# Kernel optimization log

Hardware: AMD Instinct MI355X
Metric: run time of the kernel (lower is better)

The kernel has to match this reference:

```python
import jax, jax.numpy as jnp
import numpy as np

EMB = 1024
HID = 1024
COMB = 2 * HID  # bidirectional encoder
BATCH = 16384


def _lin(x, W, b):
    # x: [B, in], W: [in, out], b: [out]
    return x @ W + b


def setup_inputs() -> dict:
    key = jax.random.key(0)
    ks = jax.random.split(key, 30)
    s = 0.02
    d = {
        "in_word": jax.random.normal(ks[0], (BATCH, EMB), jnp.float32),
        "last_hid_state": jax.random.normal(ks[1], (BATCH, HID), jnp.float32),
        "attended_state": jax.random.normal(ks[2], (BATCH, COMB), jnp.float32),
    }
    names_shapes = [
        ("W", (EMB, HID)), ("Wz", (EMB, HID)), ("Wr", (EMB, HID)),
        ("U", (HID, HID)), ("Uz", (HID, HID)), ("Ur", (HID, HID)),
        ("C", (COMB, HID)), ("Cz", (COMB, HID)), ("Cr", (COMB, HID)),
        ("Uo", (HID, HID)), ("Vo", (EMB, HID)), ("Co", (COMB, HID)),
    ]
    for i, (n, sh) in enumerate(names_shapes):
        d[n] = jax.random.normal(ks[3 + i], sh, jnp.float32) * s
        d["b" + n.lower()] = jnp.zeros((HID,), jnp.float32)
    return d


def reference(in_word, last_hid_state, attended_state,
              W, bw, Wz, bwz, Wr, bwr,
              U, bu, Uz, buz, Ur, bur,
              C, bc, Cz, bcz, Cr, bcr,
              Uo, buo, Vo, bvo, Co, bco):
    z = jax.nn.sigmoid(_lin(in_word, Wz, bwz) + _lin(last_hid_state, Uz, buz)
                       + _lin(attended_state, Cz, bcz))
    r = jax.nn.sigmoid(_lin(in_word, Wr, bwr) + _lin(last_hid_state, Ur, bur)
                       + _lin(attended_state, Cr, bcr))
    s_tilda = jnp.tanh(_lin(in_word, W, bw) + _lin(r * last_hid_state, U, bu)
                       + _lin(attended_state, C, bc))
    s = (1.0 - z) * last_hid_state + z * s_tilda
    t_i = jax.nn.relu(_lin(s, Uo, buo) + _lin(in_word, Vo, bvo)
                      + _lin(attended_state, Co, bco))
    return (s, t_i)
```

## Files before the change

kernel.cpp:

```cpp
#include <hip/hip_runtime.h>
#include <stdint.h>
#include <stddef.h>


#define MODE_Z 0
#define MODE_R 1
#define MODE_S 2
#define MODE_T 3

typedef __attribute__((ext_vector_type(8))) __bf16 bf16x8;
typedef __attribute__((ext_vector_type(4))) float f32x4;
typedef __attribute__((ext_vector_type(8))) unsigned short us8;

__device__ __forceinline__ unsigned short f2bf(float f) {
  union { float f; unsigned u; } v; v.f = f;
  unsigned r = 0x7FFFu + ((v.u >> 16) & 1u);
  return (unsigned short)((v.u + r) >> 16);
}
__device__ __forceinline__ float bf2f(unsigned short h) {
  union { unsigned u; float f; } v; v.u = ((unsigned)h) << 16;
  return v.f;
}

__device__ __forceinline__ void gload_lds16(const unsigned short* g, unsigned short* l) {
  __builtin_amdgcn_global_load_lds(
      (const __attribute__((address_space(1))) void*)g,
      (__attribute__((address_space(3))) void*)l, 16, 0, 0);
}

__global__ void cvt_xh(const float* __restrict__ x, const float* __restrict__ h,
                       unsigned short* __restrict__ xb, unsigned short* __restrict__ hb) {
  const size_t NX = 16777216;
  size_t i = ((size_t)blockIdx.x * 256 + threadIdx.x) * 8;
  const float* s; unsigned short* d; size_t off;
  if (i < NX) { s = x; d = xb; off = i; } else { s = h; d = hb; off = i - NX; }
  f32x4 v0 = *(const f32x4*)(s + off);
  f32x4 v1 = *(const f32x4*)(s + off + 4);
  us8 p = { f2bf(v0.x), f2bf(v0.y), f2bf(v0.z), f2bf(v0.w),
            f2bf(v1.x), f2bf(v1.y), f2bf(v1.z), f2bf(v1.w) };
  *(us8*)(d + off) = p;
}

__global__ void cvt_a(const float* __restrict__ a, unsigned short* __restrict__ ab) {
  size_t i = ((size_t)blockIdx.x * 256 + threadIdx.x) * 8;
  f32x4 v0 = *(const f32x4*)(a + i);
  f32x4 v1 = *(const f32x4*)(a + i + 4);
  us8 p = { f2bf(v0.x), f2bf(v0.y), f2bf(v0.z), f2bf(v0.w),
            f2bf(v1.x), f2bf(v1.y), f2bf(v1.z), f2bf(v1.w) };
  *(us8*)(ab + i) = p;
}

struct TArgs {
  const float* src[12];
  unsigned short* dst[12];
};

__global__ void transpose_all(TArgs ta) {
  __shared__ float tile[32][33];
  int t = blockIdx.x;
  int w, K, local;
  if (t < 8192) { w = t >> 10; K = 1024; local = t & 1023; }
  else { int t2 = t - 8192; w = 8 + (t2 >> 11); K = 2048; local = t2 & 2047; }
  int kb = (K == 1024) ? ((local & 31) << 5) : ((local & 63) << 5);
  int nb = (K == 1024) ? ((local >> 5) << 5) : ((local >> 6) << 5);
  const float* src = ta.src[w];
  unsigned short* dst = ta.dst[w];
  int tx = threadIdx.x, ty = threadIdx.y;
  #pragma unroll
  for (int i = 0; i < 32; i += 8)
    tile[ty + i][tx] = src[(size_t)(kb + ty + i) * 1024 + nb + tx];
  __syncthreads();
  #pragma unroll
  for (int i = 0; i < 32; i += 8)
    dst[(size_t)(nb + ty + i) * K + kb + tx] = f2bf(tile[tx][ty + i]);
}

template <int MODE>
__global__ __launch_bounds__(256, 4)
void gemm_fused(const unsigned short* __restrict__ A0,
                const unsigned short* __restrict__ A1,
                const unsigned short* __restrict__ A2,
                const unsigned short* __restrict__ B0T,
                const unsigned short* __restrict__ B1T,
                const unsigned short* __restrict__ B2T,
                const float* __restrict__ b0,
                const float* __restrict__ b1,
                const float* __restrict__ b2,
                const unsigned short* __restrict__ hb,
                const unsigned short* __restrict__ zb,
                float* __restrict__ outf,
                unsigned short* __restrict__ outb) {
  __shared__ unsigned short As[128 * 64];
  __shared__ unsigned short Bs[128 * 64];

  const int tid = threadIdx.x;
  const int bid = blockIdx.x;
  const int xcd = bid & 7;
  const int j8 = bid >> 3;
  const int mBlk = xcd * 16 + (j8 >> 3);
  const int nBlk = j8 & 7;
  const int rowBase = mBlk * 128;
  const int colBase = nBlk * 128;
  const int wave = tid >> 6;
  const int lane = tid & 63;
  const int waveM = wave >> 1;
  const int waveN = wave & 1;
  const int quad = lane >> 4;
  const int lm = lane & 15;
  const int wbase = tid & 192;

  f32x4 acc[4][4];
  #pragma unroll
  for (int i = 0; i < 4; ++i)
    #pragma unroll
    for (int j = 0; j < 4; ++j)
      acc[i][j] = (f32x4){0.f, 0.f, 0.f, 0.f};

  const unsigned short* Asegs[3] = {A0, A1, A2};
  const unsigned short* Bsegs[3] = {B0T, B1T, B2T};

  #pragma unroll
  for (int seg = 0; seg < 3; ++seg) {
    const int K = (seg == 2) ? 2048 : 1024;
    const unsigned short* Ap = Asegs[seg] + (size_t)rowBase * K;
    const unsigned short* Bp = Bsegs[seg] + (size_t)colBase * K;
    const int nChunks = K >> 6;
    for (int kc = 0; kc < nChunks; ++kc) {
      #pragma unroll
      for (int t = 0; t < 4; ++t) {
        int idx = t * 256 + tid;
        int row = idx >> 3;
        int kg = (idx & 7) ^ (row & 7);
        gload_lds16(Ap + (size_t)row * K + (kc << 6) + (kg << 3),
                    &As[(size_t)(t * 256 + wbase) << 3]);
      }
      #pragma unroll
      for (int t = 0; t < 4; ++t) {
        int idx = t * 256 + tid;
        int row = idx >> 3;
        int kg = (idx & 7) ^ (row & 7);
        gload_lds16(Bp + (size_t)row * K + (kc << 6) + (kg << 3),
                    &Bs[(size_t)(t * 256 + wbase) << 3]);
      }
      __syncthreads();
      #pragma unroll
      for (int ks = 0; ks < 2; ++ks) {
        bf16x8 av[4], bv[4];
        #pragma unroll
        for (int i = 0; i < 4; ++i) {
          int r = waveM * 64 + i * 16 + lm;
          int slot = (ks * 4 + quad) ^ (r & 7);
          av[i] = *(const bf16x8*)&As[(r << 6) + (slot << 3)];
        }
        #pragma unroll
        for (int j = 0; j < 4; ++j) {
          int c = waveN * 64 + j * 16 + lm;
          int slot = (ks * 4 + quad) ^ (c & 7);
          bv[j] = *(const bf16x8*)&Bs[(c << 6) + (slot << 3)];
        }
        #pragma unroll
        for (int i = 0; i < 4; ++i)
          #pragma unroll
          for (int j = 0; j < 4; ++j)
            acc[i][j] = __builtin_amdgcn_mfma_f32_16x16x32_bf16(av[i], bv[j], acc[i][j], 0, 0, 0);
      }
      __syncthreads();
    }
  }

  #pragma unroll
  for (int j = 0; j < 4; ++j) {
    const int col = colBase + waveN * 64 + j * 16 + lm;
    const float bias = b0[col] + b1[col] + b2[col];
    #pragma unroll
    for (int i = 0; i < 4; ++i) {
      #pragma unroll
      for (int r = 0; r < 4; ++r) {
        const int row = rowBase + waveM * 64 + i * 16 + quad * 4 + r;
        const size_t idx = (size_t)row * 1024 + col;
        float v = acc[i][j][r] + bias;
        if constexpr (MODE == MODE_Z) {
          outb[idx] = f2bf(1.f / (1.f + __expf(-v)));
        } else if constexpr (MODE == MODE_R) {
          float rv = 1.f / (1.f + __expf(-v));
          outb[idx] = f2bf(rv * bf2f(hb[idx]));
        } else if constexpr (MODE == MODE_S) {
          float avv = fabsf(v);
          float e = __expf(-2.f * avv);
          float st = (1.f - e) / (1.f + e);
          st = v < 0.f ? -st : st;
          float zv = bf2f(zb[idx]);
          float hv = bf2f(hb[idx]);
          float s = (1.f - zv) * hv + zv * st;
          outf[idx] = s;
          outb[idx] = f2bf(s);
        } else {
          outf[idx] = v > 0.f ? v : 0.f;
        }
      }
    }
  }
}

extern "C" void kernel_launch(void* const* d_in, const int* in_sizes, int n_in,
                              void* d_out, int out_size, void* d_ws, size_t ws_size,
                              hipStream_t stream) {
  (void)in_sizes; (void)n_in; (void)out_size; (void)ws_size;
  const float* x  = (const float*)d_in[0];
  const float* h  = (const float*)d_in[1];
  const float* a  = (const float*)d_in[2];
  const float* W   = (const float*)d_in[3];  const float* bw  = (const float*)d_in[4];
  const float* Wz  = (const float*)d_in[5];  const float* bwz = (const float*)d_in[6];
  const float* Wr  = (const float*)d_in[7];  const float* bwr = (const float*)d_in[8];
  const float* U   = (const float*)d_in[9];  const float* bu  = (const float*)d_in[10];
  const float* Uz  = (const float*)d_in[11]; const float* buz = (const float*)d_in[12];
  const float* Ur  = (const float*)d_in[13]; const float* bur = (const float*)d_in[14];
  const float* C   = (const float*)d_in[15]; const float* bc  = (const float*)d_in[16];
  const float* Cz  = (const float*)d_in[17]; const float* bcz = (const float*)d_in[18];
  const float* Cr  = (const float*)d_in[19]; const float* bcr = (const float*)d_in[20];
  const float* Uo  = (const float*)d_in[21]; const float* buo = (const float*)d_in[22];
  const float* Vo  = (const float*)d_in[23]; const float* bvo = (const float*)d_in[24];
  const float* Co  = (const float*)d_in[25]; const float* bco = (const float*)d_in[26];

  const size_t M1 = 1024u * 1024u;
  unsigned short* wsb = (unsigned short*)d_ws;
  unsigned short* WzT = wsb + 0 * M1;
  unsigned short* UzT = wsb + 1 * M1;
  unsigned short* WrT = wsb + 2 * M1;
  unsigned short* UrT = wsb + 3 * M1;
  unsigned short* WT  = wsb + 4 * M1;
  unsigned short* UT  = wsb + 5 * M1;
  unsigned short* VoT = wsb + 6 * M1;
  unsigned short* UoT = wsb + 7 * M1;
  unsigned short* CzT = wsb + 8 * M1;
  unsigned short* CrT = wsb + 10 * M1;
  unsigned short* CT  = wsb + 12 * M1;
  unsigned short* CoT = wsb + 14 * M1;
  unsigned short* x_bf = wsb + 16 * M1;

  unsigned short* h_bf = (unsigned short*)((float*)d_out + 16 * M1);
  unsigned short* a_bf = (unsigned short*)d_in[0];
  unsigned short* rh   = (unsigned short*)d_in[1];
  unsigned short* z_bf = (unsigned short*)d_in[1] + 16 * M1;
  unsigned short* s_bf = (unsigned short*)d_in[2];

  float* s_out = (float*)d_out;
  float* t_out = (float*)d_out + 16 * M1;

  cvt_xh<<<16384, 256, 0, stream>>>(x, h, x_bf, h_bf);
  cvt_a<<<16384, 256, 0, stream>>>(a, a_bf);
  TArgs ta;
  const float* wsrc[12] = {Wz, Uz, Wr, Ur, W, U, Vo, Uo, Cz, Cr, C, Co};
  unsigned short* wdst[12] = {WzT, UzT, WrT, UrT, WT, UT, VoT, UoT, CzT, CrT, CT, CoT};
  for (int i = 0; i < 12; ++i) { ta.src[i] = wsrc[i]; ta.dst[i] = wdst[i]; }
  transpose_all<<<16384, dim3(32, 8), 0, stream>>>(ta);

  dim3 g(1024), b(256);
  gemm_fused<MODE_R><<<g, b, 0, stream>>>(x_bf, h_bf, a_bf, WrT, UrT, CrT,
                                          bwr, bur, bcr, h_bf, nullptr, nullptr, rh);
  gemm_fused<MODE_Z><<<g, b, 0, stream>>>(x_bf, h_bf, a_bf, WzT, UzT, CzT,
                                          bwz, buz, bcz, nullptr, nullptr, nullptr, z_bf);
  gemm_fused<MODE_S><<<g, b, 0, stream>>>(x_bf, rh, a_bf, WT, UT, CT,
                                          bw, bu, bc, h_bf, z_bf, s_out, s_bf);
  gemm_fused<MODE_T><<<g, b, 0, stream>>>(x_bf, s_bf, a_bf, VoT, UoT, CoT,
                                          bvo, buo, bco, nullptr, nullptr, t_out, nullptr);
}
```

Measured before the change: 1.048 ms.

## Rewrite fused GEMM as 256x256 tile, 8-wave double-buffered pipelined kernel

Replaces the 128x128, 4-wave GEMM with a 256x256 output tile per 512-thread block. K-chunks are double-buffered in 128KB of LDS, and global-to-LDS loads for later chunks are interleaved with quadrant MFMA groups under raw s_barrier and vmcnt waits. MFMA sections are wrapped in raised wave priority. The aim is to hide load latency and raise arithmetic intensity per LDS byte. The cost is a grid of only 256 blocks at one block per CU, plus more register pressure from 128 accumulator floats per lane.

Result: slower. 1.532 ms (+46.1%).

```diff
diff --git a/kernel.cpp b/kernel.cpp
--- a/kernel.cpp
+++ b/kernel.cpp
@@ -75,8 +75,13 @@
     dst[(size_t)(nb + ty + i) * K + kb + tx] = f2bf(tile[tx][ty + i]);
 }
 
+#define BARRIER() asm volatile("s_barrier" ::: "memory")
+#define WAIT_VM(N) asm volatile("s_waitcnt vmcnt(" #N ")" ::: "memory")
+#define PRIO1() __builtin_amdgcn_s_setprio(1)
+#define PRIO0() __builtin_amdgcn_s_setprio(0)
+
 template <int MODE>
-__global__ __launch_bounds__(256, 4)
+__global__ __launch_bounds__(512, 2)
 void gemm_fused(const unsigned short* __restrict__ A0,
                 const unsigned short* __restrict__ A1,
                 const unsigned short* __restrict__ A2,
@@ -90,112 +95,161 @@
                 const unsigned short* __restrict__ zb,
                 float* __restrict__ outf,
                 unsigned short* __restrict__ outb) {
-  __shared__ unsigned short As[128 * 64];
-  __shared__ unsigned short Bs[128 * 64];
+  __shared__ unsigned short lds_s[65536];
 
   const int tid = threadIdx.x;
   const int bid = blockIdx.x;
-  const int xcd = bid & 7;
-  const int j8 = bid >> 3;
-  const int mBlk = xcd * 16 + (j8 >> 3);
-  const int nBlk = j8 & 7;
-  const int rowBase = mBlk * 128;
-  const int colBase = nBlk * 128;
-  const int wave = tid >> 6;
-  const int lane = tid & 63;
-  const int waveM = wave >> 1;
-  const int waveN = wave & 1;
-  const int quad = lane >> 4;
-  const int lm = lane & 15;
-  const int wbase = tid & 192;
-
-  f32x4 acc[4][4];
+  const int swz = (bid & 7) * 32 + (bid >> 3);
+  const int mBlk = swz >> 2;
+  const int nBlk = swz & 3;
+  const int rowBase = mBlk << 8;
+  const int colBase = nBlk << 8;
+
+  const int l = tid & 63;
+  const int w = tid >> 6;
+  const int wm = w >> 2;
+  const int wn = w & 3;
+  const int lm = l & 15;
+  const int quad = l >> 4;
+
+  f32x4 acc[4][4][2];
   #pragma unroll
-  for (int i = 0; i < 4; ++i)
-    #pragma unroll
-    for (int j = 0; j < 4; ++j)
-      acc[i][j] = (f32x4){0.f, 0.f, 0.f, 0.f};
-
-  const unsigned short* Asegs[3] = {A0, A1, A2};
-  const unsigned short* Bsegs[3] = {B0T, B1T, B2T};
+  for (int q = 0; q < 4; ++q)
+    #pragma unroll
+    for (int fr = 0; fr < 4; ++fr)
+      #pragma unroll
+      for (int fc = 0; fc < 2; ++fc)
+        acc[q][fr][fc] = (f32x4){0.f, 0.f, 0.f, 0.f};
+
+  bf16x8 aF[4][2];
+  bf16x8 bLo[2][2];
+  bf16x8 bHi[2][2];
+
+  auto STAGE = [&](int kt, int op, int half) {
+    const unsigned short* base;
+    int K, kloc;
+    if (kt < 16)      { base = op ? B0T : A0; K = 1024; kloc = kt << 6; }
+    else if (kt < 32) { base = op ? B1T : A1; K = 1024; kloc = (kt - 16) << 6; }
+    else              { base = op ? B2T : A2; K = 2048; kloc = (kt - 32) << 6; }
+    const int rb = (op ? colBase : rowBase) + (half << 7);
+    const unsigned short* g = base + (size_t)rb * K + kloc;
+    unsigned short* lb = lds_s + ((kt & 1) << 15) + (op << 14) + (half << 13);
+    #pragma unroll
+    for (int j = 0; j < 2; ++j) {
+      const int idx = (j << 9) + tid;
+      const int row = idx >> 3;
+      const int kg = (idx & 7) ^ (row & 7);
+      gload_lds16(g + (size_t)row * K + (kg << 3),
+                  lb + ((idx & ~63) << 3));
+    }
+  };
+
+  auto LOAD_A = [&](int cb, int h) {
+    #pragma unroll
+    for (int fr = 0; fr < 4; ++fr) {
+      const int r = wm * 64 + h * 128 + fr * 16 + lm;
+      #pragma unroll
+      for (int ks = 0; ks < 2; ++ks) {
+        const int slot = ((ks << 2) | quad) ^ (lm & 7);
+        aF[fr][ks] = *(const bf16x8*)(lds_s + cb + (r << 6) + (slot << 3));
+      }
+    }
+  };
+  auto LOAD_B = [&](int cb, int h, bf16x8 (&bv)[2][2]) {
+    #pragma unroll
+    for (int fc = 0; fc < 2; ++fc) {
+      const int c = wn * 32 + h * 128 + fc * 16 + lm;
+      #pragma unroll
+      for (int ks = 0; ks < 2; ++ks) {
+        const int slot = ((ks << 2) | quad) ^ (lm & 7);
+        bv[fc][ks] = *(const bf16x8*)(lds_s + cb + 16384 + (c << 6) + (slot << 3));
+      }
+    }
+  };
+  auto MFMA16 = [&](f32x4 (&aq)[4][2], bf16x8 (&bv)[2][2]) {
+    #pragma unroll
+    for (int ks = 0; ks < 2; ++ks)
+      #pragma unroll
+      for (int fr = 0; fr < 4; ++fr)
+        #pragma unroll
+        for (int fc = 0; fc < 2; ++fc)
+          aq[fr][fc] = __builtin_amdgcn_mfma_f32_16x16x32_bf16(
+              aF[fr][ks], bv[fc][ks], aq[fr][fc], 0, 0, 0);
+  };
+
+  STAGE(0, 0, 0); STAGE(0, 1, 0); STAGE(0, 1, 1); STAGE(0, 0, 1);
+  STAGE(1, 0, 0); STAGE(1, 1, 0); STAGE(1, 1, 1);
+  WAIT_VM(6);
+  BARRIER();
+
+  #pragma unroll 1
+  for (int i = 0; i < 31; ++i) {
+    const int t1 = 2 * i + 1, t2 = 2 * i + 2, t3 = 2 * i + 3;
+    LOAD_A(0, 0); LOAD_B(0, 0, bLo); STAGE(t1, 0, 1);
+    BARRIER(); PRIO1(); MFMA16(acc[0], bLo); PRIO0(); BARRIER();
+    LOAD_B(0, 1, bHi); STAGE(t2, 0, 0);
+    BARRIER(); PRIO1(); MFMA16(acc[1], bHi); PRIO0(); BARRIER();
+    LOAD_A(0, 1); STAGE(t2, 1, 0);
+    BARRIER(); PRIO1(); MFMA16(acc[2], bLo); PRIO0(); BARRIER();
+    STAGE(t2, 1, 1);
+    BARRIER(); PRIO1(); MFMA16(acc[3], bHi); PRIO0(); WAIT_VM(6); BARRIER();
+    LOAD_A(32768, 0); LOAD_B(32768, 0, bLo); STAGE(t2, 0, 1);
+    BARRIER(); PRIO1(); MFMA16(acc[0], bLo); PRIO0(); BARRIER();
+    LOAD_B(32768, 1, bHi); STAGE(t3, 0, 0);
+    BARRIER(); PRIO1(); MFMA16(acc[1], bHi); PRIO0(); BARRIER();
+    LOAD_A(32768, 1); STAGE(t3, 1, 0);
+    BARRIER(); PRIO1(); MFMA16(acc[2], bLo); PRIO0(); BARRIER();
+    STAGE(t3, 1, 1);
+    BARRIER(); PRIO1(); MFMA16(acc[3], bHi); PRIO0(); WAIT_VM(6); BARRIER();
+  }
+  LOAD_A(0, 0); LOAD_B(0, 0, bLo); STAGE(63, 0, 1);
+  BARRIER(); PRIO1(); MFMA16(acc[0], bLo); PRIO0(); BARRIER();
+  LOAD_B(0, 1, bHi);
+  BARRIER(); PRIO1(); MFMA16(acc[1], bHi); PRIO0(); BARRIER();
+  LOAD_A(0, 1);
+  BARRIER(); PRIO1(); MFMA16(acc[2], bLo); PRIO0(); BARRIER();
+  BARRIER(); PRIO1(); MFMA16(acc[3], bHi); PRIO0(); WAIT_VM(0); BARRIER();
+  LOAD_A(32768, 0); LOAD_B(32768, 0, bLo);
+  BARRIER(); PRIO1(); MFMA16(acc[0], bLo); PRIO0(); BARRIER();
+  LOAD_B(32768, 1, bHi);
+  BARRIER(); PRIO1(); MFMA16(acc[1], bHi); PRIO0(); BARRIER();
+  LOAD_A(32768, 1);
+  BARRIER(); PRIO1(); MFMA16(acc[2], bLo); PRIO0(); BARRIER();
+  BARRIER(); PRIO1(); MFMA16(acc[3], bHi); PRIO0();
 
   #pragma unroll
-  for (int seg = 0; seg < 3; ++seg) {
-    const int K = (seg == 2) ? 2048 : 1024;
-    const unsigned short* Ap = Asegs[seg] + (size_t)rowBase * K;
-    const unsigned short* Bp = Bsegs[seg] + (size_t)colBase * K;
-    const int nChunks = K >> 6;
-    for (int kc = 0; kc < nChunks; ++kc) {
-      #pragma unroll
-      for (int t = 0; t < 4; ++t) {
-        int idx = t * 256 + tid;
-        int row = idx >> 3;
-        int kg = (idx & 7) ^ (row & 7);
-        gload_lds16(Ap + (size_t)row * K + (kc << 6) + (kg << 3),
-                    &As[(size_t)(t * 256 + wbase) << 3]);
-      }
-      #pragma unroll
-      for (int t = 0; t < 4; ++t) {
-        int idx = t * 256 + tid;
-        int row = idx >> 3;
-        int kg = (idx & 7) ^ (row & 7);
-        gload_lds16(Bp + (size_t)row * K + (kc << 6) + (kg << 3),
-                    &Bs[(size_t)(t * 256 + wbase) << 3]);
-      }
-      __syncthreads();
-      #pragma unroll
-      for (int ks = 0; ks < 2; ++ks) {
-        bf16x8 av[4], bv[4];
+  for (int q = 0; q < 4; ++q) {
+    const int rQ = rowBase + wm * 64 + (q >> 1) * 128;
+    const int cQ = colBase + wn * 32 + (q & 1) * 128;
+    #pragma unroll
+    for (int fc = 0; fc < 2; ++fc) {
+      const int col = cQ + fc * 16 + lm;
+      const float bias = b0[col] + b1[col] + b2[col];
+      #pragma unroll
+      for (int fr = 0; fr < 4; ++fr) {
         #pragma unroll
-        for (int i = 0; i < 4; ++i) {
-          int r = waveM * 64 + i * 16 + lm;
-          int slot = (ks * 4 + quad) ^ (r & 7);
-          av[i] = *(const bf16x8*)&As[(r << 6) + (slot << 3)];
-        }
-        #pragma unroll
-        for (int j = 0; j < 4; ++j) {
-          int c = waveN * 64 + j * 16 + lm;
-          int slot = (ks * 4 + quad) ^ (c & 7);
-          bv[j] = *(const bf16x8*)&Bs[(c << 6) + (slot << 3)];
-        }
-        #pragma unroll
-        for (int i = 0; i < 4; ++i)
-          #pragma unroll
-          for (int j = 0; j < 4; ++j)
-            acc[i][j] = __builtin_amdgcn_mfma_f32_16x16x32_bf16(av[i], bv[j], acc[i][j], 0, 0, 0);
-      }
-      __syncthreads();
-    }
-  }
-
-  #pragma unroll
-  for (int j = 0; j < 4; ++j) {
-    const int col = colBase + waveN * 64 + j * 16 + lm;
-    const float bias = b0[col] + b1[col] + b2[col];
-    #pragma unroll
-    for (int i = 0; i < 4; ++i) {
-      #pragma unroll
-      for (int r = 0; r < 4; ++r) {
-        const int row = rowBase + waveM * 64 + i * 16 + quad * 4 + r;
-        const size_t idx = (size_t)row * 1024 + col;
-        float v = acc[i][j][r] + bias;
-        if constexpr (MODE == MODE_Z) {
-          outb[idx] = f2bf(1.f / (1.f + __expf(-v)));
-        } else if constexpr (MODE == MODE_R) {
-          float rv = 1.f / (1.f + __expf(-v));
-          outb[idx] = f2bf(rv * bf2f(hb[idx]));
-        } else if constexpr (MODE == MODE_S) {
-          float avv = fabsf(v);
-          float e = __expf(-2.f * avv);
-          float st = (1.f - e) / (1.f + e);
-          st = v < 0.f ? -st : st;
-          float zv = bf2f(zb[idx]);
-          float hv = bf2f(hb[idx]);
-          float s = (1.f - zv) * hv + zv * st;
-          outf[idx] = s;
-          outb[idx] = f2bf(s);
-        } else {
-          outf[idx] = v > 0.f ? v : 0.f;
+        for (int r = 0; r < 4; ++r) {
+          const int row = rQ + fr * 16 + quad * 4 + r;
+          const size_t idx = (size_t)row * 1024 + col;
+          float v = acc[q][fr][fc][r] + bias;
+          if constexpr (MODE == MODE_Z) {
+            outb[idx] = f2bf(1.f / (1.f + __expf(-v)));
+          } else if constexpr (MODE == MODE_R) {
+            float rv = 1.f / (1.f + __expf(-v));
+            outb[idx] = f2bf(rv * bf2f(hb[idx]));
+          } else if constexpr (MODE == MODE_S) {
+            float avv = fabsf(v);
+            float e = __expf(-2.f * avv);
+            float st = (1.f - e) / (1.f + e);
+            st = v < 0.f ? -st : st;
+            float zv = bf2f(zb[idx]);
+            float hv = bf2f(hb[idx]);
+            float s = (1.f - zv) * hv + zv * st;
+            outf[idx] = s;
+            outb[idx] = f2bf(s);
+          } else {
+            outf[idx] = v > 0.f ? v : 0.f;
+          }
         }
       }
     }
@@ -255,7 +309,7 @@
   for (int i = 0; i < 12; ++i) { ta.src[i] = wsrc[i]; ta.dst[i] = wdst[i]; }
   transpose_all<<<16384, dim3(32, 8), 0, stream>>>(ta);
 
-  dim3 g(1024), b(256);
+  dim3 g(256), b(512);
   gemm_fused<MODE_R><<<g, b, 0, stream>>>(x_bf, h_bf, a_bf, WrT, UrT, CrT,
                                           bwr, bur, bcr, h_bf, nullptr, nullptr, rh);
   gemm_fused<MODE_Z><<<g, b, 0, stream>>>(x_bf, h_bf, a_bf, WzT, UzT, CzT,
```

## Triple-buffer GEMM LDS pipeline with 128x256 tiles and 512-thread blocks

Applied to the files above, without the earlier changes.

Reworks the fused GEMM main loop into a triple-buffered software pipeline. Global-to-LDS loads for step t+2 are issued while step t computes, with explicit vmcnt/lgkmcnt waits, a single barrier per step and raised wave priority around the MFMAs. Block tiles grow to 128x256 with 8 waves and K steps of 32, so there are half as many blocks. LDS reads use an inline-asm ds_read_b128 with immediate offsets and a new XOR swizzle. The intent is to hide global load latency and cut barriers per step, at the cost of more LDS (72KB per block), which lowers occupancy, and hand-tuned waitcnt logic that is fragile.

New measurement: 1.050 ms. Within noise of the previous version (+0.2%).

```diff
diff --git a/kernel.cpp b/kernel.cpp
--- a/kernel.cpp
+++ b/kernel.cpp
@@ -26,6 +26,13 @@
   __builtin_amdgcn_global_load_lds(
       (const __attribute__((address_space(1))) void*)g,
       (__attribute__((address_space(3))) void*)l, 16, 0, 0);
+}
+
+template <int IMM>
+__device__ __forceinline__ bf16x8 dsr128i(unsigned off) {
+  bf16x8 r;
+  asm volatile("ds_read_b128 %0, %1 offset:%2" : "=v"(r) : "v"(off), "i"(IMM));
+  return r;
 }
 
 __global__ void cvt_xh(const float* __restrict__ x, const float* __restrict__ h,
@@ -75,8 +82,16 @@
     dst[(size_t)(nb + ty + i) * K + kb + tx] = f2bf(tile[tx][ty + i]);
 }
 
+#define BARRIER()     __builtin_amdgcn_s_barrier()
+#define WAIT_VM(N)    asm volatile("s_waitcnt vmcnt(" #N ")")
+#define SCHED_FENCE() __builtin_amdgcn_sched_barrier(0)
+#define WAIT_LGKM0()  do { asm volatile("s_waitcnt lgkmcnt(0)"); \
+                           __builtin_amdgcn_sched_barrier(0); } while (0)
+#define PRIO1()       __builtin_amdgcn_s_setprio(1)
+#define PRIO0()       __builtin_amdgcn_s_setprio(0)
+
 template <int MODE>
-__global__ __launch_bounds__(256, 4)
+__global__ __launch_bounds__(512, 4)
 void gemm_fused(const unsigned short* __restrict__ A0,
                 const unsigned short* __restrict__ A1,
                 const unsigned short* __restrict__ A2,
@@ -90,95 +105,124 @@
                 const unsigned short* __restrict__ zb,
                 float* __restrict__ outf,
                 unsigned short* __restrict__ outb) {
-  __shared__ unsigned short As[128 * 64];
-  __shared__ unsigned short Bs[128 * 64];
+  __shared__ unsigned short lds_s[36864];
 
   const int tid = threadIdx.x;
   const int bid = blockIdx.x;
-  const int xcd = bid & 7;
-  const int j8 = bid >> 3;
-  const int mBlk = xcd * 16 + (j8 >> 3);
-  const int nBlk = j8 & 7;
-  const int rowBase = mBlk * 128;
-  const int colBase = nBlk * 128;
-  const int wave = tid >> 6;
-  const int lane = tid & 63;
-  const int waveM = wave >> 1;
-  const int waveN = wave & 1;
-  const int quad = lane >> 4;
-  const int lm = lane & 15;
-  const int wbase = tid & 192;
+  const int swz = (bid & 7) * 64 + (bid >> 3);
+  const int mBlk = swz >> 2;
+  const int nBlk = swz & 3;
+  const int rowBase = mBlk << 7;
+  const int colBase = nBlk << 8;
+
+  const int l = tid & 63;
+  const int w = tid >> 6;
+  const int wm = w >> 2;
+  const int wn = w & 3;
+  const int lm = l & 15;
+  const int quad = l >> 4;
+
+  const unsigned slotA = (unsigned)(quad ^ ((lm >> 1) & 3));
+  const unsigned base_a = (unsigned)((wm * 64 + lm) * 64) + (slotA << 4);
+  const unsigned base_b = 8192u + (unsigned)((wn * 64 + lm) * 64) + (slotA << 4);
+
+  const int rA = tid >> 2;
+  const unsigned kg16 = (unsigned)(((tid & 3) ^ ((rA >> 1) & 3)) << 4);
+  const unsigned voA1 = (unsigned)(rowBase + rA) * 2048u + kg16;
+  const unsigned voA2 = (unsigned)(rowBase + rA) * 4096u + kg16;
+  const unsigned voB0_1 = (unsigned)(colBase + rA) * 2048u + kg16;
+  const unsigned voB1_1 = (unsigned)(colBase + 128 + rA) * 2048u + kg16;
+  const unsigned voB0_2 = (unsigned)(colBase + rA) * 4096u + kg16;
+  const unsigned voB1_2 = (unsigned)(colBase + 128 + rA) * 4096u + kg16;
 
   f32x4 acc[4][4];
   #pragma unroll
-  for (int i = 0; i < 4; ++i)
+  for (int fr = 0; fr < 4; ++fr)
     #pragma unroll
-    for (int j = 0; j < 4; ++j)
-      acc[i][j] = (f32x4){0.f, 0.f, 0.f, 0.f};
-
-  const unsigned short* Asegs[3] = {A0, A1, A2};
-  const unsigned short* Bsegs[3] = {B0T, B1T, B2T};
+    for (int fc = 0; fc < 4; ++fc)
+      acc[fr][fc] = (f32x4){0.f, 0.f, 0.f, 0.f};
+
+  auto STAGE = [&](int kt, int soff) {
+    const unsigned short *bA, *bB;
+    int tl; unsigned voA, voB0, voB1;
+    if (kt < 32)      { bA = A0; bB = B0T; tl = kt;
+                        voA = voA1; voB0 = voB0_1; voB1 = voB1_1; }
+    else if (kt < 64) { bA = A1; bB = B1T; tl = kt - 32;
+                        voA = voA1; voB0 = voB0_1; voB1 = voB1_1; }
+    else              { bA = A2; bB = B2T; tl = kt - 64;
+                        voA = voA2; voB0 = voB0_2; voB1 = voB1_2; }
+    const unsigned tb = (unsigned)(tl << 6);
+    unsigned short* ldsb = lds_s + (soff >> 1);
+    gload_lds16((const unsigned short*)((const char*)bA + voA + tb),
+                ldsb + tid * 8);
+    gload_lds16((const unsigned short*)((const char*)bB + voB0 + tb),
+                ldsb + 4096 + tid * 8);
+    gload_lds16((const unsigned short*)((const char*)bB + voB1 + tb),
+                ldsb + 8192 + tid * 8);
+  };
+
+  bf16x8 aF[4], bF[4];
+  auto READS = [&](int bufoff) {
+    const unsigned vA = (unsigned)bufoff + base_a;
+    const unsigned vB = (unsigned)bufoff + base_b;
+    aF[0] = dsr128i<0>(vA);    aF[1] = dsr128i<1024>(vA);
+    aF[2] = dsr128i<2048>(vA); aF[3] = dsr128i<3072>(vA);
+    bF[0] = dsr128i<0>(vB);    bF[1] = dsr128i<1024>(vB);
+    bF[2] = dsr128i<2048>(vB); bF[3] = dsr128i<3072>(vB);
+  };
+  auto MFMA16 = [&]() {
+    #pragma unroll
+    for (int fr = 0; fr < 4; ++fr)
+      #pragma unroll
+      for (int fc = 0; fc < 4; ++fc)
+        acc[fr][fc] = __builtin_amdgcn_mfma_f32_16x16x32_bf16(
+            aF[fr], bF[fc], acc[fr][fc], 0, 0, 0);
+  };
+
+  STAGE(0, 0);
+  STAGE(1, 24576);
+  WAIT_VM(3);
+  BARRIER(); SCHED_FENCE();
+
+  int bufoff = 0;
+  int stageoff = 49152;
+  #pragma unroll 1
+  for (int t = 0; t < 126; ++t) {
+    READS(bufoff);
+    STAGE(t + 2, stageoff);
+    WAIT_LGKM0();
+    PRIO1(); MFMA16(); PRIO0();
+    WAIT_VM(3);
+    BARRIER(); SCHED_FENCE();
+    bufoff = stageoff;
+    int nb = (bufoff == 0) ? 24576 : (bufoff == 24576 ? 49152 : 0);
+    bufoff = nb == 24576 ? 49152 : (nb == 49152 ? 0 : 24576);
+    bufoff = ((t + 1) % 3) * 24576;
+    stageoff = ((t + 3) % 3) * 24576;
+  }
+  READS(bufoff);
+  WAIT_LGKM0();
+  PRIO1(); MFMA16(); PRIO0();
+  WAIT_VM(0);
+  BARRIER(); SCHED_FENCE();
+  bufoff = (127 % 3) * 24576;
+  READS(bufoff);
+  WAIT_LGKM0();
+  PRIO1(); MFMA16(); PRIO0();
+
+  asm volatile("" ::: "memory");
 
   #pragma unroll
-  for (int seg = 0; seg < 3; ++seg) {
-    const int K = (seg == 2) ? 2048 : 1024;
-    const unsigned short* Ap = Asegs[seg] + (size_t)rowBase * K;
-    const unsigned short* Bp = Bsegs[seg] + (size_t)colBase * K;
-    const int nChunks = K >> 6;
-    for (int kc = 0; kc < nChunks; ++kc) {
-      #pragma unroll
-      for (int t = 0; t < 4; ++t) {
-        int idx = t * 256 + tid;
-        int row = idx >> 3;
-        int kg = (idx & 7) ^ (row & 7);
-        gload_lds16(Ap + (size_t)row * K + (kc << 6) + (kg << 3),
-                    &As[(size_t)(t * 256 + wbase) << 3]);
-      }
-      #pragma unroll
-      for (int t = 0; t < 4; ++t) {
-        int idx = t * 256 + tid;
-        int row = idx >> 3;
-        int kg = (idx & 7) ^ (row & 7);
-        gload_lds16(Bp + (size_t)row * K + (kc << 6) + (kg << 3),
-                    &Bs[(size_t)(t * 256 + wbase) << 3]);
-      }
-      __syncthreads();
-      #pragma unroll
-      for (int ks = 0; ks < 2; ++ks) {
-        bf16x8 av[4], bv[4];
-        #pragma unroll
-        for (int i = 0; i < 4; ++i) {
-          int r = waveM * 64 + i * 16 + lm;
-          int slot = (ks * 4 + quad) ^ (r & 7);
-          av[i] = *(const bf16x8*)&As[(r << 6) + (slot << 3)];
-        }
-        #pragma unroll
-        for (int j = 0; j < 4; ++j) {
-          int c = waveN * 64 + j * 16 + lm;
-          int slot = (ks * 4 + quad) ^ (c & 7);
-          bv[j] = *(const bf16x8*)&Bs[(c << 6) + (slot << 3)];
-        }
-        #pragma unroll
-        for (int i = 0; i < 4; ++i)
-          #pragma unroll
-          for (int j = 0; j < 4; ++j)
-            acc[i][j] = __builtin_amdgcn_mfma_f32_16x16x32_bf16(av[i], bv[j], acc[i][j], 0, 0, 0);
-      }
-      __syncthreads();
-    }
-  }
-
-  #pragma unroll
-  for (int j = 0; j < 4; ++j) {
-    const int col = colBase + waveN * 64 + j * 16 + lm;
+  for (int fc = 0; fc < 4; ++fc) {
+    const int col = colBase + wn * 64 + fc * 16 + lm;
     const float bias = b0[col] + b1[col] + b2[col];
     #pragma unroll
-    for (int i = 0; i < 4; ++i) {
+    for (int fr = 0; fr < 4; ++fr) {
       #pragma unroll
       for (int r = 0; r < 4; ++r) {
-        const int row = rowBase + waveM * 64 + i * 16 + quad * 4 + r;
+        const int row = rowBase + wm * 64 + fr * 16 + quad * 4 + r;
         const size_t idx = (size_t)row * 1024 + col;
-        float v = acc[i][j][r] + bias;
+        float v = acc[fr][fc][r] + bias;
         if constexpr (MODE == MODE_Z) {
           outb[idx] = f2bf(1.f / (1.f + __expf(-v)));
         } else if constexpr (MODE == MODE_R) {
@@ -255,7 +299,7 @@
   for (int i = 0; i < 12; ++i) { ta.src[i] = wsrc[i]; ta.dst[i] = wdst[i]; }
   transpose_all<<<16384, dim3(32, 8), 0, stream>>>(ta);
 
-  dim3 g(1024), b(256);
+  dim3 g(512), b(512);
   gemm_fused<MODE_R><<<g, b, 0, stream>>>(x_bf, h_bf, a_bf, WrT, UrT, CrT,
                                           bwr, bur, bcr, h_bf, nullptr, nullptr, rh);
   gemm_fused<MODE_Z><<<g, b, 0, stream>>>(x_bf, h_bf, a_bf, WzT, UzT, CzT,
```
